# Optimization experiments

Measured on AMD Instinct MI355X. Metric: run time of the kernel, lower is better.

Reference implementation:

```python
import jax, jax.numpy as jnp
import numpy as np

B, S, HID = 2, 2048, 1024
H, KVH, D = 16, 4, 64
N_REP = H // KVH
SCALE = D ** -0.5
CAP = 50.0


def rotate_half(x):
    x1, x2 = x[..., : D // 2], x[..., D // 2 :]
    return jnp.concatenate((-x2, x1), axis=-1)


def setup_inputs() -> dict:
    key = jax.random.key(0)
    ks = jax.random.split(key, 10)
    X = jax.random.normal(ks[0], (B, S, HID), dtype=jnp.float32)
    # RoPE tables: (B, S, D)
    inv_freq = 1.0 / (10000.0 ** (np.arange(0, D, 2, dtype=np.float32) / D))
    pos = np.arange(S, dtype=np.float32)
    freqs = np.outer(pos, inv_freq)  # (S, D/2)
    emb = np.concatenate([freqs, freqs], axis=-1)  # (S, D)
    cos = jnp.broadcast_to(jnp.asarray(np.cos(emb)), (B, S, D))
    sin = jnp.broadcast_to(jnp.asarray(np.sin(emb)), (B, S, D))
    # causal mask: 1 where key <= query
    mask = jnp.broadcast_to(jnp.tril(jnp.ones((S, S), dtype=jnp.int32)), (B, S, S))
    std = HID ** -0.5
    Wq = jax.random.normal(ks[1], (HID, HID), dtype=jnp.float32) * std
    bq = jnp.zeros((HID,), dtype=jnp.float32)
    Wk = jax.random.normal(ks[2], (KVH * D, HID), dtype=jnp.float32) * std
    bk = jnp.zeros((KVH * D,), dtype=jnp.float32)
    Wv = jax.random.normal(ks[3], (KVH * D, HID), dtype=jnp.float32) * std
    bv = jnp.zeros((KVH * D,), dtype=jnp.float32)
    Wo = jax.random.normal(ks[4], (HID, HID), dtype=jnp.float32) * std
    bo = jnp.zeros((HID,), dtype=jnp.float32)
    return {"X": X, "cos": cos, "sin": sin, "mask": mask,
            "Wq": Wq, "bq": bq, "Wk": Wk, "bk": bk,
            "Wv": Wv, "bv": bv, "Wo": Wo, "bo": bo}


def reference(X, cos, sin, mask, Wq, bq, Wk, bk, Wv, bv, Wo, bo):
    bsz, q_len, _ = X.shape
    q = (X @ Wq.T + bq).reshape(bsz, q_len, H, D).transpose(0, 2, 1, 3)    # (B,H,S,D)
    k = (X @ Wk.T + bk).reshape(bsz, q_len, KVH, D).transpose(0, 2, 1, 3)  # (B,KVH,S,D)
    v = (X @ Wv.T + bv).reshape(bsz, q_len, KVH, D).transpose(0, 2, 1, 3)
    c = cos[:, None, :, :]  # (B,1,S,D)
    s = sin[:, None, :, :]
    q = q * c + rotate_half(q) * s
    k = k * c + rotate_half(k) * s
    k = jnp.repeat(k, N_REP, axis=1)  # GQA expand -> (B,H,S,D)
    v = jnp.repeat(v, N_REP, axis=1)
    scores = jnp.einsum('bhqd,bhkd->bhqk', q, k) * SCALE
    scores = jnp.clip(scores, -CAP, CAP)  # attention cap
    scores = jnp.where(mask[:, None, :, :] == 0, -1e9, scores)
    attn = jax.nn.softmax(scores, axis=-1)  # dropout p=0 -> identity
    ctx = jnp.einsum('bhqk,bhkd->bhqd', attn, v)
    ctx = ctx.transpose(0, 2, 1, 3).reshape(bsz, q_len, H * D)
    out = ctx @ Wo.T + bo
    return (out, attn)
```

## Files before the change

### kernel.cpp

```cpp
#include <hip/hip_runtime.h>
#include <cstdint>
#include <cstddef>

#define S_LEN   2048
#define BATCH   2
#define HID_DIM 1024
#define NHEAD   16
#define NKV     4
#define DHEAD   64
#define SCALE_F 0.125f
#define L2E     1.44269504f
#define QSCALE  (SCALE_F * L2E)
#define CAPL2   (50.0f * L2E)

typedef unsigned short u16;
typedef __attribute__((ext_vector_type(8))) short  short8_t;
typedef __attribute__((ext_vector_type(4))) float  f32x4;
typedef __attribute__((ext_vector_type(4))) u16    u16x4;

static __device__ __forceinline__ u16 f2bf(float f) {
  uint32_t x = __builtin_bit_cast(uint32_t, f);
  x += 0x7fffu + ((x >> 16) & 1u);
  return (u16)(x >> 16);
}

static __device__ __forceinline__ void gload_lds16(const void* g, void* l) {
  __builtin_amdgcn_global_load_lds((const __attribute__((address_space(1))) void*)g,
                                   (__attribute__((address_space(3))) void*)l, 16, 0, 0);
}

static __device__ __forceinline__ float exp2med3(float x) {
  return __builtin_amdgcn_exp2f(__builtin_amdgcn_fmed3f(x, -CAPL2, CAPL2));
}

static __device__ __forceinline__ short8_t pack8(f32x4 a, f32x4 b) {
  short8_t r;
  r[0] = (short)f2bf(a[0]); r[1] = (short)f2bf(a[1]);
  r[2] = (short)f2bf(a[2]); r[3] = (short)f2bf(a[3]);
  r[4] = (short)f2bf(b[0]); r[5] = (short)f2bf(b[1]);
  r[6] = (short)f2bf(b[2]); r[7] = (short)f2bf(b[3]);
  return r;
}

__global__ void cast_all(const float* __restrict__ X,  u16* __restrict__ xb,
                         const float* __restrict__ Wq, u16* __restrict__ wqb,
                         const float* __restrict__ Wk, u16* __restrict__ wkb,
                         const float* __restrict__ Wv, u16* __restrict__ wvb,
                         const float* __restrict__ Wo, u16* __restrict__ wob) {
  const float* src; u16* dst; int n4;
  switch (blockIdx.y) {
    case 0:  src = X;  dst = xb;  n4 = (BATCH * S_LEN * HID_DIM) / 4; break;
    case 1:  src = Wq; dst = wqb; n4 = (HID_DIM * HID_DIM) / 4;       break;
    case 2:  src = Wk; dst = wkb; n4 = (NKV * DHEAD * HID_DIM) / 4;   break;
    case 3:  src = Wv; dst = wvb; n4 = (NKV * DHEAD * HID_DIM) / 4;   break;
    default: src = Wo; dst = wob; n4 = (HID_DIM * HID_DIM) / 4;       break;
  }
  for (int i = blockIdx.x * 256 + threadIdx.x; i < n4; i += gridDim.x * 256) {
    f32x4 v = ((const f32x4*)src)[i];
    u16x4 o;
    o[0] = f2bf(v[0]); o[1] = f2bf(v[1]); o[2] = f2bf(v[2]); o[3] = f2bf(v[3]);
    ((u16x4*)dst)[i] = o;
  }
}

__global__ __launch_bounds__(256, 4) void gemm_qkv(const u16* __restrict__ Xb,
                                                   const u16* __restrict__ Wqb,
                                                   const u16* __restrict__ Wkb,
                                                   const u16* __restrict__ Wvb,
                                                   const float* __restrict__ bq,
                                                   const float* __restrict__ bk,
                                                   const float* __restrict__ bv,
                                                   const float* __restrict__ cosb,
                                                   const float* __restrict__ sinb,
                                                   u16* __restrict__ qout,
                                                   u16* __restrict__ kout,
                                                   u16* __restrict__ vtout) {
  __shared__ u16 As[64 * 64];
  __shared__ u16 Bs[128 * 64];
  const int tid = threadIdx.x, lane = tid & 63, wid = tid >> 6;
  const int l15 = lane & 15, lg = lane >> 4;
  const int m0 = blockIdx.x * 64, n0 = blockIdx.y * 128;
  const int wm = wid & 1, wn = wid >> 1;
  const int K = HID_DIM;

  const u16* Wp; const float* biasp; int nl, mode;
  if (n0 < 1024)      { Wp = Wqb; biasp = bq; nl = n0;        mode = 0; }
  else if (n0 < 1280) { Wp = Wkb; biasp = bk; nl = n0 - 1024; mode = 1; }
  else                { Wp = Wvb; biasp = bv; nl = n0 - 1280; mode = 2; }

  f32x4 acc[4][2];
  #pragma unroll
  for (int a = 0; a < 4; ++a)
    #pragma unroll
    for (int b2 = 0; b2 < 2; ++b2) acc[a][b2] = (f32x4){0.f, 0.f, 0.f, 0.f};

  const int srow = (lane >> 3), sg = (lane & 7);

  for (int kk = 0; kk < K; kk += 64) {
    __syncthreads();
    #pragma unroll
    for (int i = 0; i < 6; ++i) {
      const int c = wid * 6 + i;
      if (c < 8) {
        const int r = c * 8 + srow;
        const int g = sg ^ (r & 7);
        gload_lds16(Xb + (size_t)(m0 + r) * K + kk + g * 8, As + c * 512);
      } else {
        const int cb = c - 8;
        const int r = cb * 8 + srow;
        const int g = sg ^ (r & 7);
        gload_lds16(Wp + (size_t)(nl + r) * K + kk + g * 8, Bs + cb * 512);
      }
    }
    __syncthreads();
    #pragma unroll
    for (int ks = 0; ks < 2; ++ks) {
      short8_t xa[2], wb[4];
      #pragma unroll
      for (int f = 0; f < 2; ++f) {
        const int rm = wm * 32 + f * 16 + l15;
        xa[f] = *(const short8_t*)(As + rm * 64 + (((ks * 4 + lg) ^ (rm & 7)) * 8));
      }
      #pragma unroll
      for (int f = 0; f < 4; ++f) {
        const int rn = wn * 64 + f * 16 + l15;
        wb[f] = *(const short8_t*)(Bs + rn * 64 + (((ks * 4 + lg) ^ (rn & 7)) * 8));
      }
      if (mode != 2) {
        #pragma unroll
        for (int fn = 0; fn < 4; ++fn)
          #pragma unroll
          for (int fm = 0; fm < 2; ++fm)
            acc[fn][fm] = __builtin_amdgcn_mfma_f32_16x16x32_bf16(wb[fn], xa[fm], acc[fn][fm], 0, 0, 0);
      } else {
        #pragma unroll
        for (int fn = 0; fn < 4; ++fn)
          #pragma unroll
          for (int fm = 0; fm < 2; ++fm)
            acc[fn][fm] = __builtin_amdgcn_mfma_f32_16x16x32_bf16(xa[fm], wb[fn], acc[fn][fm], 0, 0, 0);
      }
    }
  }

  const int m_base = m0 + wm * 32;
  const int nlb = nl + wn * 64;

  if (mode < 2) {
    const int Nout = (mode == 0) ? HID_DIM : (NKV * DHEAD);
    const float qs = (mode == 0) ? QSCALE : 1.0f;
    u16* outb = (mode == 0) ? qout : kout;
    #pragma unroll
    for (int fm = 0; fm < 2; ++fm) {
      const int row = m_base + fm * 16 + l15;
      #pragma unroll
      for (int fn = 0; fn < 2; ++fn) {
        const int dh = fn * 16 + lg * 4;
        const f32x4 c4 = *(const f32x4*)(cosb + (size_t)row * 64 + dh);
        const f32x4 s4 = *(const f32x4*)(sinb + (size_t)row * 64 + dh);
        f32x4 x1 = acc[fn][fm]     + *(const f32x4*)(biasp + nlb + fn * 16 + lg * 4);
        f32x4 x2 = acc[fn + 2][fm] + *(const f32x4*)(biasp + nlb + (fn + 2) * 16 + lg * 4);
        f32x4 o1 = (x1 * c4 - x2 * s4) * qs;
        f32x4 o2 = (x2 * c4 + x1 * s4) * qs;
        u16x4 u1, u2;
        #pragma unroll
        for (int i = 0; i < 4; ++i) { u1[i] = f2bf(o1[i]); u2[i] = f2bf(o2[i]); }
        *(u16x4*)(outb + (size_t)row * Nout + nlb + fn * 16 + lg * 4)       = u1;
        *(u16x4*)(outb + (size_t)row * Nout + nlb + (fn + 2) * 16 + lg * 4) = u2;
      }
    }
  } else {
    #pragma unroll
    for (int fn = 0; fn < 4; ++fn) {
      const int d = nlb + fn * 16 + l15;
      const float bvs = biasp[d];
      #pragma unroll
      for (int fm = 0; fm < 2; ++fm) {
        const int s0 = m_base + fm * 16 + lg * 4;
        const int b_ = s0 >> 11, s_ = s0 & (S_LEN - 1);
        u16x4 o;
        #pragma unroll
        for (int i = 0; i < 4; ++i) o[i] = f2bf(acc[fn][fm][i] + bvs);
        *(u16x4*)(vtout + (size_t)(b_ * 256 + d) * S_LEN + s_) = o;
      }
    }
  }
}

__global__ __launch_bounds__(256, 4) void gemm_out(const u16* __restrict__ A,
                                                   const u16* __restrict__ W,
                                                   const float* __restrict__ bias,
                                                   float* __restrict__ outp) {
  __shared__ u16 As[64 * 64];
  __shared__ u16 Bs[128 * 64];
  const int tid = threadIdx.x, lane = tid & 63, wid = tid >> 6;
  const int l15 = lane & 15, lg = lane >> 4;
  const int m0 = blockIdx.x * 64, n0 = blockIdx.y * 128;
  const int wm = wid & 1, wn = wid >> 1;
  const int K = HID_DIM, N = HID_DIM;

  f32x4 acc[4][2];
  #pragma unroll
  for (int a = 0; a < 4; ++a)
    #pragma unroll
    for (int b2 = 0; b2 < 2; ++b2) acc[a][b2] = (f32x4){0.f, 0.f, 0.f, 0.f};

  const int srow = (lane >> 3), sg = (lane & 7);

  for (int kk = 0; kk < K; kk += 64) {
    __syncthreads();
    #pragma unroll
    for (int i = 0; i < 6; ++i) {
      const int c = wid * 6 + i;
      if (c < 8) {
        const int r = c * 8 + srow;
        const int g = sg ^ (r & 7);
        gload_lds16(A + (size_t)(m0 + r) * K + kk + g * 8, As + c * 512);
      } else {
        const int cb = c - 8;
        const int r = cb * 8 + srow;
        const int g = sg ^ (r & 7);
        gload_lds16(W + (size_t)(n0 + r) * K + kk + g * 8, Bs + cb * 512);
      }
    }
    __syncthreads();
    #pragma unroll
    for (int ks = 0; ks < 2; ++ks) {
      short8_t xa[2], wb[4];
      #pragma unroll
      for (int f = 0; f < 2; ++f) {
        const int rm = wm * 32 + f * 16 + l15;
        xa[f] = *(const short8_t*)(As + rm * 64 + (((ks * 4 + lg) ^ (rm & 7)) * 8));
      }
      #pragma unroll
      for (int f = 0; f < 4; ++f) {
        const int rn = wn * 64 + f * 16 + l15;
        wb[f] = *(const short8_t*)(Bs + rn * 64 + (((ks * 4 + lg) ^ (rn & 7)) * 8));
      }
      #pragma unroll
      for (int fn = 0; fn < 4; ++fn)
        #pragma unroll
        for (int fm = 0; fm < 2; ++fm)
          acc[fn][fm] = __builtin_amdgcn_mfma_f32_16x16x32_bf16(wb[fn], xa[fm], acc[fn][fm], 0, 0, 0);
    }
  }

  const int m_base = m0 + wm * 32, n_base = n0 + wn * 64;
  #pragma unroll
  for (int fn = 0; fn < 4; ++fn) {
    const int col = n_base + fn * 16 + lg * 4;
    const f32x4 bvv = *(const f32x4*)(bias + col);
    #pragma unroll
    for (int fm = 0; fm < 2; ++fm) {
      const int row = m_base + fm * 16 + l15;
      *(f32x4*)(outp + (size_t)row * N + col) = acc[fn][fm] + bvv;
    }
  }
}

__global__ __launch_bounds__(256, 4) void attn_fused(const u16* __restrict__ qb,
                                                     const u16* __restrict__ kb,
                                                     const u16* __restrict__ vtb,
                                                     float* __restrict__ attn,
                                                     u16* __restrict__ ctxb) {
  __shared__ __attribute__((aligned(16))) char smem[40960];

  const int tid = threadIdx.x, lane = tid & 63, wid = tid >> 6;
  const int l15 = lane & 15, lg = lane >> 4;
  const int bh = blockIdx.x, b = bh >> 4, h = bh & 15, kvh = h >> 2;
  const int qt = (int)(gridDim.y - 1 - blockIdx.y);
  const int q0 = qt * 64;
  const int NT = qt + 1;
  const int qw = q0 + wid * 16;
  const int qrow = qw + l15;

  const u16* qp = qb + (size_t)(b * S_LEN + qrow) * HID_DIM + h * DHEAD + lg * 8;
  const short8_t qf0 = *(const short8_t*)qp;
  const short8_t qf1 = *(const short8_t*)(qp + 32);

  const u16* kbase  = kb  + (size_t)(b * S_LEN) * (NKV * DHEAD) + kvh * DHEAD;
  const u16* vtbase = vtb + (size_t)(b * NKV + kvh) * DHEAD * S_LEN;

  const int sr8 = wid * 8 + (lane >> 3);
  const int sgr = lane & 7;

  {
    u16* kb0 = (u16*)smem;
    u16* kb1 = (u16*)(smem + 16384);
    const int NT2 = (qt + 2) >> 1;

    auto stageK128 = [&](u16* dst, int kv0) {
      #pragma unroll
      for (int it = 0; it < 4; ++it) {
        const int r = it * 32 + sr8;
        const int g = sgr ^ (r & 7);
        gload_lds16(kbase + (size_t)(kv0 + r) * (NKV * DHEAD) + g * 8,
                    dst + (it * 32 + wid * 8) * 64);
      }
    };

    f32x4 lacc = (f32x4){0.f, 0.f, 0.f, 0.f};
    stageK128(kb0, 0);
    for (int t = 0; t < NT2; ++t) {
      const int kv0 = t * 128;
      if (t + 1 < NT2) {
        stageK128((t & 1) ? kb0 : kb1, kv0 + 128);
        asm volatile("s_waitcnt vmcnt(4)" ::: "memory");
      } else {
        asm volatile("s_waitcnt vmcnt(0)" ::: "memory");
      }
      __builtin_amdgcn_s_barrier();
      const u16* ks = (t & 1) ? kb1 : kb0;
      const bool maskc = (kv0 + 127 > qw);
      #pragma unroll
      for (int g16 = 0; g16 < 8; ++g16) {
        const int r = g16 * 16 + l15;
        short8_t ka0 = *(const short8_t*)(ks + r * 64 + ((lg ^ (r & 7)) * 8));
        short8_t ka1 = *(const short8_t*)(ks + r * 64 + (((4 + lg) ^ (r & 7)) * 8));
        f32x4 sacc = (f32x4){0.f, 0.f, 0.f, 0.f};
        sacc = __builtin_amdgcn_mfma_f32_16x16x32_bf16(ka0, qf0, sacc, 0, 0, 0);
        sacc = __builtin_amdgcn_mfma_f32_16x16x32_bf16(ka1, qf1, sacc, 0, 0, 0);
        #pragma unroll
        for (int i = 0; i < 4; ++i) {
          float e = exp2med3(sacc[i]);
          if (maskc) {
            const int kvi = kv0 + g16 * 16 + lg * 4 + i;
            e = (kvi <= qrow) ? e : 0.f;
          }
          lacc[i] += e;
        }
      }
      __builtin_amdgcn_s_barrier();
    }
    float lsum_ = (lacc[0] + lacc[1]) + (lacc[2] + lacc[3]);
    lsum_ += __shfl_xor(lsum_, 16);
    lsum_ += __shfl_xor(lsum_, 32);
    const float invl = 1.f / lsum_;

    u16* kS2a = (u16*)smem;
    u16* kS2b = (u16*)(smem + 8192);
    u16* vS   = (u16*)(smem + 16384);
    float (*pF)[64] = (float(*)[64])(smem + 24576 + wid * 4096);

    auto stageK = [&](u16* dst, int kv0) {
      #pragma unroll
      for (int it = 0; it < 2; ++it) {
        const int r = it * 32 + sr8;
        const int g = sgr ^ (r & 7);
        gload_lds16(kbase + (size_t)(kv0 + r) * (NKV * DHEAD) + g * 8,
                    dst + (it * 32 + wid * 8) * 64);
      }
    };
    auto stageV = [&](int kv0) {
      #pragma unroll
      for (int it = 0; it < 2; ++it) {
        const int r = it * 32 + sr8;
        const int g = sgr ^ (r & 7);
        gload_lds16(vtbase + (size_t)r * S_LEN + kv0 + g * 8,
                    vS + (it * 32 + wid * 8) * 64);
      }
    };

    float* abase = attn + (size_t)bh * S_LEN * S_LEN;
    f32x4 ctx[4];
    #pragma unroll
    for (int dt = 0; dt < 4; ++dt) ctx[dt] = (f32x4){0.f, 0.f, 0.f, 0.f};

    const int r2 = lane >> 4, c16 = lane & 15;

    stageK(kS2a, 0);
    asm volatile("s_waitcnt vmcnt(0)" ::: "memory");
    __builtin_amdgcn_s_barrier();

    for (int t = 0; t < NT; ++t) {
      const int kv0 = t * 64;
      stageV(kv0);
      const bool pre = (t + 1 < NT);
      if (pre) stageK((t & 1) ? kS2a : kS2b, kv0 + 64);

      const u16* ks = (t & 1) ? kS2b : kS2a;
      const bool maskc = (kv0 + 63 > qw);
      #pragma unroll
      for (int g16 = 0; g16 < 4; ++g16) {
        const int r = g16 * 16 + l15;
        short8_t ka0 = *(const short8_t*)(ks + r * 64 + ((lg ^ (r & 7)) * 8));
        short8_t ka1 = *(const short8_t*)(ks + r * 64 + (((4 + lg) ^ (r & 7)) * 8));
        f32x4 sacc = (f32x4){0.f, 0.f, 0.f, 0.f};
        sacc = __builtin_amdgcn_mfma_f32_16x16x32_bf16(ka0, qf0, sacc, 0, 0, 0);
        sacc = __builtin_amdgcn_mfma_f32_16x16x32_bf16(ka1, qf1, sacc, 0, 0, 0);
        f32x4 pv;
        #pragma unroll
        for (int i = 0; i < 4; ++i) {
          float p = exp2med3(sacc[i]) * invl;
          if (maskc) {
            const int kvi = kv0 + g16 * 16 + lg * 4 + i;
            p = (kvi <= qrow) ? p : 0.f;
          }
          pv[i] = p;
        }
        *(f32x4*)&pF[l15][((g16 * 4 + lg) ^ l15) * 4] = pv;
      }

      #pragma unroll
      for (int j = 0; j < 4; ++j) {
        const int R = j * 4 + r2;
        f32x4 v = *(const f32x4*)&pF[R][(c16 ^ R) * 4];
        *(f32x4*)(abase + (size_t)(qw + R) * S_LEN + kv0 + c16 * 4) = v;
      }

      if (pre) asm volatile("s_waitcnt vmcnt(6)" ::: "memory");
      else     asm volatile("s_waitcnt vmcnt(4)" ::: "memory");
      __builtin_amdgcn_s_barrier();

      f32x4 alo = *(const f32x4*)&pF[l15][((2 * lg) ^ l15) * 4];
      f32x4 ahi = *(const f32x4*)&pF[l15][((2 * lg + 1) ^ l15) * 4];
      f32x4 blo = *(const f32x4*)&pF[l15][((8 + 2 * lg) ^ l15) * 4];
      f32x4 bhi = *(const f32x4*)&pF[l15][((9 + 2 * lg) ^ l15) * 4];
      short8_t pa0 = pack8(alo, ahi);
      short8_t pa1 = pack8(blo, bhi);
      #pragma unroll
      for (int dt = 0; dt < 4; ++dt) {
        const int r = dt * 16 + l15;
        short8_t bv0 = *(const short8_t*)(vS + r * 64 + ((lg ^ (r & 7)) * 8));
        short8_t bv1 = *(const short8_t*)(vS + r * 64 + (((4 + lg) ^ (r & 7)) * 8));
        ctx[dt] = __builtin_amdgcn_mfma_f32_16x16x32_bf16(bv0, pa0, ctx[dt], 0, 0, 0);
        ctx[dt] = __builtin_amdgcn_mfma_f32_16x16x32_bf16(bv1, pa1, ctx[dt], 0, 0, 0);
      }

      if (pre) {
        asm volatile("s_waitcnt vmcnt(4)" ::: "memory");
        __builtin_amdgcn_s_barrier();
      }
    }

    #pragma unroll
    for (int dt = 0; dt < 4; ++dt) {
      u16x4 o;
      #pragma unroll
      for (int i = 0; i < 4; ++i) o[i] = f2bf(ctx[dt][i]);
      *(u16x4*)(ctxb + (size_t)(b * S_LEN + qrow) * HID_DIM + h * DHEAD + dt * 16 + lg * 4) = o;
    }

    const int zc0 = q0 + 64;
    if (zc0 < S_LEN) {
      const f32x4 z = (f32x4){0.f, 0.f, 0.f, 0.f};
      for (int r = wid; r < 64; r += 4) {
        float* rowp = abase + (size_t)(q0 + r) * S_LEN;
        for (int c = zc0 + lane * 4; c < S_LEN; c += 256)
          *(f32x4*)(rowp + c) = z;
      }
    }
  }
}

extern "C" void kernel_launch(void* const* d_in, const int* in_sizes, int n_in,
                              void* d_out, int out_size, void* d_ws, size_t ws_size,
                              hipStream_t stream) {
  (void)in_sizes; (void)n_in; (void)out_size; (void)ws_size;
  const float* X    = (const float*)d_in[0];
  const float* cosb = (const float*)d_in[1];
  const float* sinb = (const float*)d_in[2];
  const float* Wq = (const float*)d_in[4];
  const float* bq = (const float*)d_in[5];
  const float* Wk = (const float*)d_in[6];
  const float* bk = (const float*)d_in[7];
  const float* Wv = (const float*)d_in[8];
  const float* bv = (const float*)d_in[9];
  const float* Wo = (const float*)d_in[10];
  const float* bo = (const float*)d_in[11];

  float* outp  = (float*)d_out;
  float* attnp = outp + (size_t)BATCH * S_LEN * HID_DIM;

  const int M = BATCH * S_LEN;
  u16* ws    = (u16*)d_ws;
  u16* Xb    = ws;
  u16* Wqb   = Xb  + (size_t)M * HID_DIM;
  u16* Wkb   = Wqb + (size_t)HID_DIM * HID_DIM;
  u16* Wvb   = Wkb + (size_t)NKV * DHEAD * HID_DIM;
  u16* Wob   = Wvb + (size_t)NKV * DHEAD * HID_DIM;
  u16* qbuf  = Wob + (size_t)HID_DIM * HID_DIM;
  u16* kbuf  = qbuf + (size_t)M * HID_DIM;
  u16* vtbuf = kbuf + (size_t)M * NKV * DHEAD;
  u16* ctxb  = vtbuf + (size_t)M * NKV * DHEAD;

  cast_all<<<dim3(1024, 5), 256, 0, stream>>>(X, Xb, Wq, Wqb, Wk, Wkb, Wv, Wvb, Wo, Wob);

  gemm_qkv<<<dim3(M / 64, 12), 256, 0, stream>>>(Xb, Wqb, Wkb, Wvb, bq, bk, bv,
                                                 cosb, sinb, qbuf, kbuf, vtbuf);

  attn_fused<<<dim3(BATCH * NHEAD, S_LEN / 64), 256, 0, stream>>>(qbuf, kbuf, vtbuf, attnp, ctxb);

  gemm_out<<<dim3(M / 64, HID_DIM / 128), 256, 0, stream>>>(ctxb, Wob, bo, outp);
}
```

Baseline: 209.3 us.

## Make softmax-denominator pass per-wave with private K buffers, hoist zero-fill earlier

The first pass, which computes the row sums, now has each wave stage its own 32-row K tiles into a private double buffer. Each wave loops only up to its own causal limit, which removes block-wide barriers and skips tiles beyond that wave's rows. The zero-fill of the masked upper part of the attention matrix moves before the second pass so its stores can overlap with later work. In exchange each wave loads K redundantly, since K is no longer shared across the block, and the tiles are smaller.

```diff
diff --git a/kernel.cpp b/kernel.cpp
--- a/kernel.cpp
+++ b/kernel.cpp
@@ -280,42 +280,39 @@
   const u16* kbase  = kb  + (size_t)(b * S_LEN) * (NKV * DHEAD) + kvh * DHEAD;
   const u16* vtbase = vtb + (size_t)(b * NKV + kvh) * DHEAD * S_LEN;
 
-  const int sr8 = wid * 8 + (lane >> 3);
-  const int sgr = lane & 7;
-
+  float* abase = attn + (size_t)bh * S_LEN * S_LEN;
+
+  f32x4 lacc = (f32x4){0.f, 0.f, 0.f, 0.f};
   {
-    u16* kb0 = (u16*)smem;
-    u16* kb1 = (u16*)(smem + 16384);
-    const int NT2 = (qt + 2) >> 1;
-
-    auto stageK128 = [&](u16* dst, int kv0) {
-      #pragma unroll
-      for (int it = 0; it < 4; ++it) {
-        const int r = it * 32 + sr8;
-        const int g = sgr ^ (r & 7);
-        gload_lds16(kbase + (size_t)(kv0 + r) * (NKV * DHEAD) + g * 8,
-                    dst + (it * 32 + wid * 8) * 64);
+    u16* myb0 = (u16*)(smem + wid * 8192);
+    u16* myb1 = myb0 + 2048;
+
+    auto stage32 = [&](u16* dst, int kv0) {
+      #pragma unroll
+      for (int i = 0; i < 4; ++i) {
+        const int r = i * 8 + (lane >> 3);
+        const int g = (lane & 7) ^ (r & 7);
+        gload_lds16(kbase + (size_t)(kv0 + r) * (NKV * DHEAD) + g * 8, dst + i * 512);
       }
     };
 
-    f32x4 lacc = (f32x4){0.f, 0.f, 0.f, 0.f};
-    stageK128(kb0, 0);
-    for (int t = 0; t < NT2; ++t) {
-      const int kv0 = t * 128;
-      if (t + 1 < NT2) {
-        stageK128((t & 1) ? kb0 : kb1, kv0 + 128);
+    const int myNT = (qw >> 5) + 1;
+    stage32(myb0, 0);
+    for (int t = 0; t < myNT; ++t) {
+      const int kv0 = t * 32;
+      u16* cur = (t & 1) ? myb1 : myb0;
+      if (t + 1 < myNT) {
+        stage32((t & 1) ? myb0 : myb1, kv0 + 32);
         asm volatile("s_waitcnt vmcnt(4)" ::: "memory");
       } else {
         asm volatile("s_waitcnt vmcnt(0)" ::: "memory");
       }
-      __builtin_amdgcn_s_barrier();
-      const u16* ks = (t & 1) ? kb1 : kb0;
-      const bool maskc = (kv0 + 127 > qw);
-      #pragma unroll
-      for (int g16 = 0; g16 < 8; ++g16) {
+      const bool maskc = (kv0 + 31 > qw);
+      #pragma unroll
+      for (int g16 = 0; g16 < 2; ++g16) {
         const int r = g16 * 16 + l15;
-        short8_t ka0 = *(const short8_t*)(ks + r * 64 + ((lg ^ (r & 7)) * 8));
-        short8_t ka1 = *(const short8_t*)(ks + r * 64 + (((4 + lg) ^ (r & 7)) * 8));
+        short8_t ka0 = *(const short8_t*)(cur + r * 64 + ((lg ^ (r & 7)) * 8));
+        short8_t ka1 = *(const short8_t*)(cur + r * 64 + (((4 + lg) ^ (r & 7)) * 8));
         f32x4 sacc = (f32x4){0.f, 0.f, 0.f, 0.f};
         sacc = __builtin_amdgcn_mfma_f32_16x16x32_bf16(ka0, qf0, sacc, 0, 0, 0);
         sacc = __builtin_amdgcn_mfma_f32_16x16x32_bf16(ka1, qf1, sacc, 0, 0, 0);
@@ -329,126 +326,129 @@
           lacc[i] += e;
         }
       }
+    }
+  }
+  float lsum = (lacc[0] + lacc[1]) + (lacc[2] + lacc[3]);
+  lsum += __shfl_xor(lsum, 16);
+  lsum += __shfl_xor(lsum, 32);
+  const float invl = 1.f / lsum;
+
+  const int zc0 = q0 + 64;
+  if (zc0 < S_LEN) {
+    const f32x4 z = (f32x4){0.f, 0.f, 0.f, 0.f};
+    for (int r = wid; r < 64; r += 4) {
+      float* rowp = abase + (size_t)(q0 + r) * S_LEN;
+      for (int c = zc0 + lane * 4; c < S_LEN; c += 256)
+        *(f32x4*)(rowp + c) = z;
+    }
+  }
+
+  __builtin_amdgcn_s_barrier();
+
+  u16* kS0 = (u16*)smem;
+  u16* kS1 = (u16*)(smem + 8192);
+  u16* vS  = (u16*)(smem + 16384);
+  float (*pF)[64] = (float(*)[64])(smem + 24576 + wid * 4096);
+
+  const int sr8 = wid * 8 + (lane >> 3);
+  const int sgr = lane & 7;
+
+  auto stageK = [&](u16* dst, int kv0) {
+    #pragma unroll
+    for (int it = 0; it < 2; ++it) {
+      const int r = it * 32 + sr8;
+      const int g = sgr ^ (r & 7);
+      gload_lds16(kbase + (size_t)(kv0 + r) * (NKV * DHEAD) + g * 8,
+                  dst + (it * 32 + wid * 8) * 64);
+    }
+  };
+  auto stageV = [&](int kv0) {
+    #pragma unroll
+    for (int it = 0; it < 2; ++it) {
+      const int r = it * 32 + sr8;
+      const int g = sgr ^ (r & 7);
+      gload_lds16(vtbase + (size_t)r * S_LEN + kv0 + g * 8,
+                  vS + (it * 32 + wid * 8) * 64);
+    }
+  };
+
+  f32x4 ctx[4];
+  #pragma unroll
+  for (int dt = 0; dt < 4; ++dt) ctx[dt] = (f32x4){0.f, 0.f, 0.f, 0.f};
+
+  const int r2 = lane >> 4, c16 = lane & 15;
+
+  stageK(kS0, 0);
+  asm volatile("s_waitcnt vmcnt(0)" ::: "memory");
+  __builtin_amdgcn_s_barrier();
+
+  for (int t = 0; t < NT; ++t) {
+    const int kv0 = t * 64;
+    stageV(kv0);
+    const bool pre = (t + 1 < NT);
+    if (pre) stageK((t & 1) ? kS0 : kS1, kv0 + 64);
+
+    const u16* ks = (t & 1) ? kS1 : kS0;
+    const bool maskc = (kv0 + 63 > qw);
+    #pragma unroll
+    for (int g16 = 0; g16 < 4; ++g16) {
+      const int r = g16 * 16 + l15;
+      short8_t ka0 = *(const short8_t*)(ks + r * 64 + ((lg ^ (r & 7)) * 8));
+      short8_t ka1 = *(const short8_t*)(ks + r * 64 + (((4 + lg) ^ (r & 7)) * 8));
+      f32x4 sacc = (f32x4){0.f, 0.f, 0.f, 0.f};
+      sacc = __builtin_amdgcn_mfma_f32_16x16x32_bf16(ka0, qf0, sacc, 0, 0, 0);
+      sacc = __builtin_amdgcn_mfma_f32_16x16x32_bf16(ka1, qf1, sacc, 0, 0, 0);
+      f32x4 pv;
+      #pragma unroll
+      for (int i = 0; i < 4; ++i) {
+        float p = exp2med3(sacc[i]) * invl;
+        if (maskc) {
+          const int kvi = kv0 + g16 * 16 + lg * 4 + i;
+          p = (kvi <= qrow) ? p : 0.f;
+        }
+        pv[i] = p;
+      }
+      *(f32x4*)&pF[l15][((g16 * 4 + lg) ^ l15) * 4] = pv;
+    }
+
+    #pragma unroll
+    for (int j = 0; j < 4; ++j) {
+      const int R = j * 4 + r2;
+      f32x4 v = *(const f32x4*)&pF[R][(c16 ^ R) * 4];
+      *(f32x4*)(abase + (size_t)(qw + R) * S_LEN + kv0 + c16 * 4) = v;
+    }
+
+    if (pre) asm volatile("s_waitcnt vmcnt(6)" ::: "memory");
+    else     asm volatile("s_waitcnt vmcnt(4)" ::: "memory");
+    __builtin_amdgcn_s_barrier();
+
+    f32x4 alo = *(const f32x4*)&pF[l15][((2 * lg) ^ l15) * 4];
+    f32x4 ahi = *(const f32x4*)&pF[l15][((2 * lg + 1) ^ l15) * 4];
+    f32x4 blo = *(const f32x4*)&pF[l15][((8 + 2 * lg) ^ l15) * 4];
+    f32x4 bhi = *(const f32x4*)&pF[l15][((9 + 2 * lg) ^ l15) * 4];
+    short8_t pa0 = pack8(alo, ahi);
+    short8_t pa1 = pack8(blo, bhi);
+    #pragma unroll
+    for (int dt = 0; dt < 4; ++dt) {
+      const int r = dt * 16 + l15;
+      short8_t bv0 = *(const short8_t*)(vS + r * 64 + ((lg ^ (r & 7)) * 8));
+      short8_t bv1 = *(const short8_t*)(vS + r * 64 + (((4 + lg) ^ (r & 7)) * 8));
+      ctx[dt] = __builtin_amdgcn_mfma_f32_16x16x32_bf16(bv0, pa0, ctx[dt], 0, 0, 0);
+      ctx[dt] = __builtin_amdgcn_mfma_f32_16x16x32_bf16(bv1, pa1, ctx[dt], 0, 0, 0);
+    }
+
+    if (pre) {
+      asm volatile("s_waitcnt vmcnt(4)" ::: "memory");
       __builtin_amdgcn_s_barrier();
     }
-    float lsum_ = (lacc[0] + lacc[1]) + (lacc[2] + lacc[3]);
-    lsum_ += __shfl_xor(lsum_, 16);
-    lsum_ += __shfl_xor(lsum_, 32);
-    const float invl = 1.f / lsum_;
-
-    u16* kS2a = (u16*)smem;
-    u16* kS2b = (u16*)(smem + 8192);
-    u16* vS   = (u16*)(smem + 16384);
-    float (*pF)[64] = (float(*)[64])(smem + 24576 + wid * 4096);
-
-    auto stageK = [&](u16* dst, int kv0) {
-      #pragma unroll
-      for (int it = 0; it < 2; ++it) {
-        const int r = it * 32 + sr8;
-        const int g = sgr ^ (r & 7);
-        gload_lds16(kbase + (size_t)(kv0 + r) * (NKV * DHEAD) + g * 8,
-                    dst + (it * 32 + wid * 8) * 64);
-      }
-    };
-    auto stageV = [&](int kv0) {
-      #pragma unroll
-      for (int it = 0; it < 2; ++it) {
-        const int r = it * 32 + sr8;
-        const int g = sgr ^ (r & 7);
-        gload_lds16(vtbase + (size_t)r * S_LEN + kv0 + g * 8,
-                    vS + (it * 32 + wid * 8) * 64);
-      }
-    };
-
-    float* abase = attn + (size_t)bh * S_LEN * S_LEN;
-    f32x4 ctx[4];
-    #pragma unroll
-    for (int dt = 0; dt < 4; ++dt) ctx[dt] = (f32x4){0.f, 0.f, 0.f, 0.f};
-
-    const int r2 = lane >> 4, c16 = lane & 15;
-
-    stageK(kS2a, 0);
-    asm volatile("s_waitcnt vmcnt(0)" ::: "memory");
-    __builtin_amdgcn_s_barrier();
-
-    for (int t = 0; t < NT; ++t) {
-      const int kv0 = t * 64;
-      stageV(kv0);
-      const bool pre = (t + 1 < NT);
-      if (pre) stageK((t & 1) ? kS2a : kS2b, kv0 + 64);
-
-      const u16* ks = (t & 1) ? kS2b : kS2a;
-      const bool maskc = (kv0 + 63 > qw);
-      #pragma unroll
-      for (int g16 = 0; g16 < 4; ++g16) {
-        const int r = g16 * 16 + l15;
-        short8_t ka0 = *(const short8_t*)(ks + r * 64 + ((lg ^ (r & 7)) * 8));
-        short8_t ka1 = *(const short8_t*)(ks + r * 64 + (((4 + lg) ^ (r & 7)) * 8));
-        f32x4 sacc = (f32x4){0.f, 0.f, 0.f, 0.f};
-        sacc = __builtin_amdgcn_mfma_f32_16x16x32_bf16(ka0, qf0, sacc, 0, 0, 0);
-        sacc = __builtin_amdgcn_mfma_f32_16x16x32_bf16(ka1, qf1, sacc, 0, 0, 0);
-        f32x4 pv;
-        #pragma unroll
-        for (int i = 0; i < 4; ++i) {
-          float p = exp2med3(sacc[i]) * invl;
-          if (maskc) {
-            const int kvi = kv0 + g16 * 16 + lg * 4 + i;
-            p = (kvi <= qrow) ? p : 0.f;
-          }
-          pv[i] = p;
-        }
-        *(f32x4*)&pF[l15][((g16 * 4 + lg) ^ l15) * 4] = pv;
-      }
-
-      #pragma unroll
-      for (int j = 0; j < 4; ++j) {
-        const int R = j * 4 + r2;
-        f32x4 v = *(const f32x4*)&pF[R][(c16 ^ R) * 4];
-        *(f32x4*)(abase + (size_t)(qw + R) * S_LEN + kv0 + c16 * 4) = v;
-      }
-
-      if (pre) asm volatile("s_waitcnt vmcnt(6)" ::: "memory");
-      else     asm volatile("s_waitcnt vmcnt(4)" ::: "memory");
-      __builtin_amdgcn_s_barrier();
-
-      f32x4 alo = *(const f32x4*)&pF[l15][((2 * lg) ^ l15) * 4];
-      f32x4 ahi = *(const f32x4*)&pF[l15][((2 * lg + 1) ^ l15) * 4];
-      f32x4 blo = *(const f32x4*)&pF[l15][((8 + 2 * lg) ^ l15) * 4];
-      f32x4 bhi = *(const f32x4*)&pF[l15][((9 + 2 * lg) ^ l15) * 4];
-      short8_t pa0 = pack8(alo, ahi);
-      short8_t pa1 = pack8(blo, bhi);
-      #pragma unroll
-      for (int dt = 0; dt < 4; ++dt) {
-        const int r = dt * 16 + l15;
-        short8_t bv0 = *(const short8_t*)(vS + r * 64 + ((lg ^ (r & 7)) * 8));
-        short8_t bv1 = *(const short8_t*)(vS + r * 64 + (((4 + lg) ^ (r & 7)) * 8));
-        ctx[dt] = __builtin_amdgcn_mfma_f32_16x16x32_bf16(bv0, pa0, ctx[dt], 0, 0, 0);
-        ctx[dt] = __builtin_amdgcn_mfma_f32_16x16x32_bf16(bv1, pa1, ctx[dt], 0, 0, 0);
-      }
-
-      if (pre) {
-        asm volatile("s_waitcnt vmcnt(4)" ::: "memory");
-        __builtin_amdgcn_s_barrier();
-      }
-    }
-
-    #pragma unroll
-    for (int dt = 0; dt < 4; ++dt) {
-      u16x4 o;
-      #pragma unroll
-      for (int i = 0; i < 4; ++i) o[i] = f2bf(ctx[dt][i]);
-      *(u16x4*)(ctxb + (size_t)(b * S_LEN + qrow) * HID_DIM + h * DHEAD + dt * 16 + lg * 4) = o;
-    }
-
-    const int zc0 = q0 + 64;
-    if (zc0 < S_LEN) {
-      const f32x4 z = (f32x4){0.f, 0.f, 0.f, 0.f};
-      for (int r = wid; r < 64; r += 4) {
-        float* rowp = abase + (size_t)(q0 + r) * S_LEN;
-        for (int c = zc0 + lane * 4; c < S_LEN; c += 256)
-          *(f32x4*)(rowp + c) = z;
-      }
-    }
+  }
+
+  #pragma unroll
+  for (int dt = 0; dt < 4; ++dt) {
+    u16x4 o;
+    #pragma unroll
+    for (int i = 0; i < 4; ++i) o[i] = f2bf(ctx[dt][i]);
+    *(u16x4*)(ctxb + (size_t)(b * S_LEN + qrow) * HID_DIM + h * DHEAD + dt * 16 + lg * 4) = o;
   }
 }
 
```

Result: slower. 213.7 us (+2.1%).
